# Kernel tuning notes

Hardware: AMD Instinct MI355X
Metric: run time of the kernel (lower is better)

Reference implementation:

```python
import jax, jax.numpy as jnp
import numpy as np

B, H, W = 16, 16, 16
DIM = 768
NH = 8
HD = DIM // NH
NEXP = 8
TOPK = 2
DSTATE = 1
DTRANK = 4
KDIR = 4


def setup_inputs() -> dict:
    key = jax.random.key(0)
    ks = jax.random.split(key, 16)
    s = 1.0 / float(np.sqrt(DIM))
    inp = {
        'x': jax.random.normal(ks[0], (B, H, W, DIM)),
        'sa_in_w': jax.random.normal(ks[1], (3 * DIM, DIM)) * s,
        'sa_in_b': jnp.zeros((3 * DIM,)),
        'sa_out_w': jax.random.normal(ks[2], (DIM, DIM)) * s,
        'sa_out_b': jnp.zeros((DIM,)),
        'ca_in_w': jax.random.normal(ks[3], (2 * DIM, DIM)) * s,
        'ca_in_b': jnp.zeros((2 * DIM,)),
        'expert_queries': jax.random.normal(ks[4], (NEXP, DIM)) * s,
        'e_in_w': jax.random.normal(ks[5], (NEXP, 2 * DIM, DIM)) * s,
        'e_in_b': jnp.zeros((NEXP, 2 * DIM)),
        'e_conv_w': jax.random.normal(ks[6], (NEXP, DIM, 1, 3, 3)) / 3.0,
        'e_conv_b': jnp.zeros((NEXP, DIM)),
        'e_xproj_w': jax.random.normal(ks[7], (NEXP, KDIR, DTRANK + 2 * DSTATE, DIM)) * s,
        'e_dtproj_w': jax.random.normal(ks[8], (NEXP, KDIR, DIM, DTRANK)) * 0.1,
        'e_dtproj_b': jax.random.uniform(ks[9], (NEXP, KDIR, DIM), minval=-4.0, maxval=-2.0),
        'e_Alog': jax.random.uniform(ks[10], (NEXP, KDIR, DIM, DSTATE), minval=0.0, maxval=1.0),
        'e_D': jnp.ones((NEXP, KDIR, DIM)),
        'e_ln_scale': jnp.ones((NEXP, DIM)),
        'e_ln_bias': jnp.zeros((NEXP, DIM)),
    }
    return {k: v.astype(jnp.float32) for k, v in inp.items()}


def _selective_scan(xs, Wx, Wdt, bdt, Alog, D):
    # xs: [B, L, d]; Wx: [R+2N, d]; Wdt: [d, R]; Alog: [d, N]; D: [d]
    dbl = jnp.einsum('bld,ed->ble', xs, Wx)
    dt = jax.nn.softplus(jnp.einsum('blr,dr->bld', dbl[..., :DTRANK], Wdt) + bdt)
    Bm = dbl[..., DTRANK:DTRANK + DSTATE]
    Cm = dbl[..., DTRANK + DSTATE:]
    A = -jnp.exp(Alog)  # [d, N]

    def step(h, t):
        dt_t, B_t, C_t, x_t = t  # [b,d],[b,N],[b,N],[b,d]
        h = jnp.exp(dt_t[:, :, None] * A) * h + (dt_t * x_t)[:, :, None] * B_t[:, None, :]
        return h, jnp.einsum('bdn,bn->bd', h, C_t)

    b, L, d = xs.shape
    h0 = jnp.zeros((b, d, DSTATE), xs.dtype)
    tm = lambda a: jnp.moveaxis(a, 1, 0)
    _, ys = jax.lax.scan(step, h0, (tm(dt), tm(Bm), tm(Cm), tm(xs)))
    return jnp.moveaxis(ys, 0, 1) + D * xs


def _expert(in_w, in_b, conv_w, conv_b, xproj_w, dtp_w, dtp_b, Alog, D, ln_s, ln_b, x):
    b = x.shape[0]
    xz = jnp.einsum('bhwc,oc->bhwo', x, in_w) + in_b
    xc, z = jnp.split(xz, 2, axis=-1)
    xn = jax.lax.conv_general_dilated(jnp.transpose(xc, (0, 3, 1, 2)), conv_w,
                                      (1, 1), ((1, 1), (1, 1)), feature_group_count=DIM)
    xc = jax.nn.silu(jnp.transpose(xn + conv_b[None, :, None, None], (0, 2, 3, 1)))
    L = H * W
    xh = xc.reshape(b, L, DIM)                              # row-major 'h'
    xv = jnp.transpose(xc, (0, 2, 1, 3)).reshape(b, L, DIM)  # col-major 'v'
    seqs = jnp.stack([xh, xh[:, ::-1], xv, xv[:, ::-1]])     # [4, b, L, d]
    ys = jax.vmap(_selective_scan)(seqs, xproj_w, dtp_w, dtp_b, Alog, D)
    yv = ys[2] + ys[3][:, ::-1]
    yv = jnp.transpose(yv.reshape(b, W, H, DIM), (0, 2, 1, 3)).reshape(b, L, DIM)
    y = (ys[0] + ys[1][:, ::-1] + yv).reshape(b, H, W, DIM)
    mu = y.mean(-1, keepdims=True)
    var = ((y - mu) ** 2).mean(-1, keepdims=True)
    y = (y - mu) * jax.lax.rsqrt(var + 1e-5) * ln_s + ln_b   # out_norm (LayerNorm)
    y = y * jax.nn.silu(z)
    return y.mean((1, 2))  # AdaptiveAvgPool2d((1,1)) -> [b, DIM]


def _forward(x, sa_in_w, sa_in_b, sa_out_w, sa_out_b, ca_in_w, ca_in_b, expert_queries,
             e_in_w, e_in_b, e_conv_w, e_conv_b, e_xproj_w, e_dtproj_w, e_dtproj_b,
             e_Alog, e_D, e_ln_scale, e_ln_bias):
    b = x.shape[0]
    L = H * W
    scale = 1.0 / float(np.sqrt(HD))
    xs = x.reshape(b, L, DIM)
    # spatial self-attention (eval mode: dropout off)
    qkv = xs @ sa_in_w.T + sa_in_b
    q, k, v = [a.reshape(b, L, NH, HD) for a in jnp.split(qkv, 3, -1)]
    att = jax.nn.softmax(jnp.einsum('bqhd,bkhd->bhqk', q, k) * scale, -1)
    ctx = jnp.einsum('bhqk,bkhd->bqhd', att, v).reshape(b, L, DIM) @ sa_out_w.T + sa_out_b
    # expert cross-attention: only head-averaged attention weights are used
    q2 = (ctx @ ca_in_w[:DIM].T + ca_in_b[:DIM]).reshape(b, L, NH, HD)
    k2 = (expert_queries @ ca_in_w[DIM:].T + ca_in_b[DIM:]).reshape(NEXP, NH, HD)
    aw = jax.nn.softmax(jnp.einsum('blhd,ehd->bhle', q2, k2) * scale, -1).mean(1)  # [b,L,E]
    gate = jax.nn.softmax(aw.mean(1), -1)  # [b, E]
    tk_scores, tk_idx = jax.lax.top_k(gate, TOPK)
    wgt = jax.nn.softmax(tk_scores, -1)
    # dense expert compute (all experts on all samples), then gather top-k
    all_out = jax.vmap(_expert, in_axes=(0,) * 11 + (None,))(
        e_in_w, e_in_b, e_conv_w, e_conv_b, e_xproj_w, e_dtproj_w, e_dtproj_b,
        e_Alog, e_D, e_ln_scale, e_ln_bias, x)  # [E, b, DIM]
    per_b = jnp.transpose(all_out, (1, 0, 2))  # [b, E, DIM]
    sel = jnp.take_along_axis(per_b, tk_idx[:, :, None], axis=1)  # [b, K, DIM]
    return jnp.sum(wgt[:, :, None] * sel, axis=1)  # [b, DIM]


def reference(x, sa_in_w, sa_in_b, sa_out_w, sa_out_b, ca_in_w, ca_in_b, expert_queries,
              e_in_w, e_in_b, e_conv_w, e_conv_b, e_xproj_w, e_dtproj_w, e_dtproj_b,
              e_Alog, e_D, e_ln_scale, e_ln_bias):
    return _forward(x, sa_in_w, sa_in_b, sa_out_w, sa_out_b, ca_in_w, ca_in_b, expert_queries,
                    e_in_w, e_in_b, e_conv_w, e_conv_b, e_xproj_w, e_dtproj_w, e_dtproj_b,
                    e_Alog, e_D, e_ln_scale, e_ln_bias)
```

## Files before the change

kernel.cpp:

```cpp
#include <hip/hip_runtime.h>
#include <hip/hip_bf16.h>


#define LTOK 256
#define DIMC 768

typedef unsigned short ushortt;
typedef __attribute__((ext_vector_type(8))) short bf16x8;
typedef __attribute__((ext_vector_type(4))) float f32x4;

#define LOG2E 1.44269504f
#define LN2   0.69314718f

__device__ __forceinline__ float fexp2(float x) { return __builtin_amdgcn_exp2f(x); }
__device__ __forceinline__ float flog2(float x) { return __builtin_amdgcn_logf(x); }

__device__ __forceinline__ ushortt f2b(float f) {
  union { float f; unsigned u; } c; c.f = f;
  unsigned r = (c.u + 0x7FFFu + ((c.u >> 16) & 1u)) >> 16;
  return (ushortt)r;
}

__global__ __launch_bounds__(256) void mk_mcast4(
    const float* __restrict__ s0, ushortt* __restrict__ d0,
    const float* __restrict__ s1, ushortt* __restrict__ d1,
    const float* __restrict__ s2, ushortt* __restrict__ d2,
    const float* __restrict__ s3, ushortt* __restrict__ d3)
{
  long g = (long)blockIdx.x * 256 + threadIdx.x;
  const float* s; ushortt* dst; long o;
  if (g < 786432)       { s = s0; dst = d0; o = g; }
  else if (g < 1228800) { s = s1; dst = d1; o = g - 786432; }
  else if (g < 1376256) { s = s2; dst = d2; o = g - 1228800; }
  else                  { s = s3; dst = d3; o = g - 1376256; }
  o <<= 2;
  float4 v = *(const float4*)(s + o);
  ushort4 w;
  w.x = f2b(v.x); w.y = f2b(v.y); w.z = f2b(v.z); w.w = f2b(v.w);
  *(ushort4*)(dst + o) = w;
}

__global__ __launch_bounds__(256) void mk_cast(const float* __restrict__ in,
                                               ushortt* __restrict__ outp, long n)
{
  long i = ((long)blockIdx.x * 256 + threadIdx.x) * 4;
  if (i + 3 < n) {
    float4 v = *(const float4*)(in + i);
    ushort4 o;
    o.x = f2b(v.x); o.y = f2b(v.y); o.z = f2b(v.z); o.w = f2b(v.w);
    *(ushort4*)(outp + i) = o;
  }
}

__global__ __launch_bounds__(256) void mk_mfma(
    const ushortt* __restrict__ A, const ushortt* __restrict__ B,
    const float* __restrict__ bias, void* __restrict__ C,
    int K, int lda, int ldb, int ldc,
    int zdiv, long sA1, long sA2, long sB1, long sB2, long sC1, long sC2,
    long sBias,
    const int* __restrict__ pairExp, int tilesN,
    int outBf, int splitN, void* __restrict__ C2, int ldc2, int outBf2, int c2vt)
{
  int z = blockIdx.y;
  long aoff, boff, coff, biasoff = 0;
  if (pairExp) {
    int e = pairExp[z];
    aoff = (long)(z >> 1) * sA1; boff = (long)e * sB1;
    coff = (long)z * sC1; biasoff = (long)e * sBias;
  } else {
    int z1 = z / zdiv, z2 = z - z1 * zdiv;
    aoff = (long)z1 * sA1 + (long)z2 * sA2;
    boff = (long)z1 * sB1 + (long)z2 * sB2;
    coff = (long)z1 * sC1 + (long)z2 * sC2;
  }
  int tile = blockIdx.x;
  int tm = tile / tilesN, tn = tile - tm * tilesN;
  long m0 = (long)tm << 7, n0 = (long)tn << 7;

  __shared__ ushortt As[128][40];
  __shared__ ushortt Bs[128][40];

  int tid = threadIdx.x;
  int lane = tid & 63, wvi = tid >> 6;
  int wr = wvi >> 1, wc = wvi & 1;
  int lm = lane & 15, lg = lane >> 4;

  f32x4 zero4 = {0.f, 0.f, 0.f, 0.f};
  f32x4 acc[4][4];
#pragma unroll
  for (int i = 0; i < 4; i++)
#pragma unroll
    for (int j = 0; j < 4; j++) acc[i][j] = zero4;

  const ushortt* Ab = A + aoff;
  const ushortt* Bb = B + boff;

  for (int k0 = 0; k0 < K; k0 += 32) {
#pragma unroll
    for (int h = 0; h < 2; h++) {
      int q = tid + h * 256;
      int row = q >> 2, ck = (q & 3) << 3;
      *(uint4*)&As[row][ck] = *(const uint4*)(Ab + (m0 + row) * lda + k0 + ck);
      *(uint4*)&Bs[row][ck] = *(const uint4*)(Bb + (n0 + row) * ldb + k0 + ck);
    }
    __syncthreads();
    bf16x8 af[4], bfr[4];
#pragma unroll
    for (int i = 0; i < 4; i++)
      af[i] = *(const bf16x8*)&As[wr * 64 + i * 16 + lm][lg << 3];
#pragma unroll
    for (int j = 0; j < 4; j++)
      bfr[j] = *(const bf16x8*)&Bs[wc * 64 + j * 16 + lm][lg << 3];
#pragma unroll
    for (int i = 0; i < 4; i++)
#pragma unroll
      for (int j = 0; j < 4; j++)
        acc[i][j] = __builtin_amdgcn_mfma_f32_16x16x32_bf16(af[i], bfr[j], acc[i][j], 0, 0, 0);
    __syncthreads();
  }

#pragma unroll
  for (int mt = 0; mt < 4; mt++) {
#pragma unroll
    for (int nt = 0; nt < 4; nt++) {
      long grow = m0 + wr * 64 + mt * 16 + lg * 4;
      long gcol = n0 + wc * 64 + nt * 16 + lm;
      float bv = bias ? bias[biasoff + gcol] : 0.f;
      if ((int)gcol < splitN) {
#pragma unroll
        for (int r = 0; r < 4; r++) {
          float v = acc[mt][nt][r] + bv;
          long idx = coff + (grow + r) * ldc + gcol;
          if (outBf) ((ushortt*)C)[idx] = f2b(v);
          else ((float*)C)[idx] = v;
        }
      } else if (c2vt) {
        int cc = (int)gcol - splitN;
        int hh = cc / 96, jj = cc - hh * 96;
#pragma unroll
        for (int r = 0; r < 4; r++) {
          float v = acc[mt][nt][r] + bv;
          long gr = grow + r;
          long b = gr >> 8, t = gr & 255;
          long idx = (((b * 8 + hh) * 128 + jj) << 8) + t;
          ((ushortt*)C2)[idx] = f2b(v);
        }
      } else {
        long col = gcol - splitN;
#pragma unroll
        for (int r = 0; r < 4; r++) {
          float v = acc[mt][nt][r] + bv;
          long idx = coff + (grow + r) * ldc2 + col;
          if (outBf2) ((ushortt*)C2)[idx] = f2b(v);
          else ((float*)C2)[idx] = v;
        }
      }
    }
  }
}

__global__ __launch_bounds__(256) void mk_gemm(
    const float* __restrict__ A, const float* __restrict__ B,
    const float* __restrict__ bias, float* __restrict__ C,
    int M, int N, int K, int lda, int ldb, int ldc, int tilesN)
{
  int tile = blockIdx.x;
  int tm = tile / tilesN, tn = tile - tm * tilesN;
  int m0 = tm << 6, n0 = tn << 6;

  __shared__ float As[16][68];
  __shared__ float Bs[16][68];

  int tid = threadIdx.x;
  int tx = tid & 15, ty = tid >> 4;
  int lrow = tid >> 2;
  int lk = (tid & 3) << 2;

  float acc[4][4];
#pragma unroll
  for (int i = 0; i < 4; i++)
#pragma unroll
    for (int j = 0; j < 4; j++) acc[i][j] = 0.f;

  for (int k0 = 0; k0 < K; k0 += 16) {
    {
      int gm = m0 + lrow;
      float4 v = {0.f, 0.f, 0.f, 0.f};
      if (gm < M) v = *(const float4*)(A + (long)gm * lda + (k0 + lk));
      As[lk + 0][lrow] = v.x; As[lk + 1][lrow] = v.y;
      As[lk + 2][lrow] = v.z; As[lk + 3][lrow] = v.w;
    }
    {
      int gn = n0 + lrow;
      float4 v = {0.f, 0.f, 0.f, 0.f};
      if (gn < N) v = *(const float4*)(B + (long)gn * ldb + (k0 + lk));
      Bs[lk + 0][lrow] = v.x; Bs[lk + 1][lrow] = v.y;
      Bs[lk + 2][lrow] = v.z; Bs[lk + 3][lrow] = v.w;
    }
    __syncthreads();
#pragma unroll
    for (int kk = 0; kk < 16; kk++) {
      float4 a = *(const float4*)&As[kk][ty << 2];
      float4 b = *(const float4*)&Bs[kk][tx << 2];
      acc[0][0] += a.x * b.x; acc[0][1] += a.x * b.y; acc[0][2] += a.x * b.z; acc[0][3] += a.x * b.w;
      acc[1][0] += a.y * b.x; acc[1][1] += a.y * b.y; acc[1][2] += a.y * b.z; acc[1][3] += a.y * b.w;
      acc[2][0] += a.z * b.x; acc[2][1] += a.z * b.y; acc[2][2] += a.z * b.z; acc[2][3] += a.z * b.w;
      acc[3][0] += a.w * b.x; acc[3][1] += a.w * b.y; acc[3][2] += a.w * b.z; acc[3][3] += a.w * b.w;
    }
    __syncthreads();
  }

#pragma unroll
  for (int i = 0; i < 4; i++) {
    int gm = m0 + (ty << 2) + i;
    if (gm >= M) continue;
#pragma unroll
    for (int j = 0; j < 4; j++) {
      int gn = n0 + (tx << 2) + j;
      if (gn >= N) continue;
      float v = acc[i][j];
      if (bias) v += bias[gn];
      C[(long)gm * ldc + gn] = v;
    }
  }
}

__global__ __launch_bounds__(256) void mk_softmax(const float* __restrict__ scores,
                                                  ushortt* __restrict__ att, float scale)
{
  int row = (blockIdx.x << 2) + (threadIdx.x >> 6);
  int lane = threadIdx.x & 63;
  const float* p = scores + (long)row * 256 + (lane << 2);
  float4 v = *(const float4*)p;
  float m = fmaxf(fmaxf(v.x, v.y), fmaxf(v.z, v.w));
#pragma unroll
  for (int o = 32; o; o >>= 1) m = fmaxf(m, __shfl_xor(m, o, 64));
  float sl = scale * LOG2E;
  v.x = fexp2(sl * (v.x - m));
  v.y = fexp2(sl * (v.y - m));
  v.z = fexp2(sl * (v.z - m));
  v.w = fexp2(sl * (v.w - m));
  float s = v.x + v.y + v.z + v.w;
#pragma unroll
  for (int o = 32; o; o >>= 1) s += __shfl_xor(s, o, 64);
  float r = 1.f / s;
  ushort4 o4;
  o4.x = f2b(v.x * r); o4.y = f2b(v.y * r); o4.z = f2b(v.z * r); o4.w = f2b(v.w * r);
  *(ushort4*)(att + (long)row * 256 + (lane << 2)) = o4;
}

__global__ __launch_bounds__(256) void mk_gates(const float* __restrict__ q2,
                                                const float* __restrict__ k2,
                                                float* __restrict__ gacc)
{
  __shared__ float k2p[8 * 808];
  int b = blockIdx.x >> 4, q = blockIdx.x & 15;
  for (int i = threadIdx.x; i < 6144; i += 256) {
    int e = i / 768, rem = i - e * 768;
    int h = rem / 96, j = rem - h * 96;
    k2p[e * 808 + h * 100 + j] = k2[i];
  }
  __syncthreads();
  const float scale = 0.10206207261596577f;
  int wid = threadIdx.x >> 6, lane = threadIdx.x & 63;
  int h = lane >> 3, e = lane & 7;
  const float* kp = &k2p[e * 808 + h * 100];
  float accL = 0.f;
#pragma unroll
  for (int ti = 0; ti < 4; ti++) {
    int l = q * 16 + wid * 4 + ti;
    const float* qh = q2 + ((long)b * LTOK + l) * DIMC + h * 96;
    float sum = 0.f;
#pragma unroll
    for (int j = 0; j < 96; j += 4) {
      float4 qv = *(const float4*)(qh + j);
      float4 kv = *(const float4*)(kp + j);
      sum += qv.x * kv.x + qv.y * kv.y + qv.z * kv.z + qv.w * kv.w;
    }
    float s = sum * scale;
    float mx = s;
#pragma unroll
    for (int o = 1; o <= 4; o <<= 1) mx = fmaxf(mx, __shfl_xor(mx, o, 64));
    float ex = fexp2((s - mx) * LOG2E);
    float se = ex;
#pragma unroll
    for (int o = 1; o <= 4; o <<= 1) se += __shfl_xor(se, o, 64);
    accL += ex / se;
  }
#pragma unroll
  for (int o = 8; o <= 32; o <<= 1) accL += __shfl_xor(accL, o, 64);
  __shared__ float red[4][8];
  if (lane < 8) red[wid][lane] = accL;
  __syncthreads();
  if (threadIdx.x < 8) {
    float v = red[0][threadIdx.x] + red[1][threadIdx.x] +
              red[2][threadIdx.x] + red[3][threadIdx.x];
    atomicAdd(&gacc[b * 8 + threadIdx.x], v);
  }
}

__global__ __launch_bounds__(64) void mk_gatetop(const float* __restrict__ gacc,
                                                 int* __restrict__ pe,
                                                 float* __restrict__ pw)
{
  int b = threadIdx.x;
  if (b >= 16) return;
  float g[8];
  for (int e = 0; e < 8; e++) g[e] = gacc[b * 8 + e] * (1.f / (8.f * 256.f));
  float mx = g[0];
  for (int e = 1; e < 8; e++) mx = fmaxf(mx, g[e]);
  float se = 0.f;
  for (int e = 0; e < 8; e++) { g[e] = expf(g[e] - mx); se += g[e]; }
  for (int e = 0; e < 8; e++) g[e] /= se;
  int i0 = 0;
  for (int e = 1; e < 8; e++) if (g[e] > g[i0]) i0 = e;
  int i1 = (i0 == 0) ? 1 : 0;
  for (int e = 0; e < 8; e++) if (e != i0 && g[e] > g[i1]) i1 = e;
  float w0 = 1.f / (1.f + expf(g[i1] - g[i0]));
  pe[2 * b] = i0; pe[2 * b + 1] = i1;
  pw[2 * b] = w0; pw[2 * b + 1] = 1.f - w0;
}

__global__ __launch_bounds__(768) void mk_conv(const float* __restrict__ xzx,
                                               const float* __restrict__ cw,
                                               const float* __restrict__ cb,
                                               const int* __restrict__ pe,
                                               float* __restrict__ xc)
{
  int blk = blockIdx.x;
  int p = blk >> 8, t = blk & 255;
  int e = pe[p];
  int h = t >> 4, w = t & 15;
  int c = threadIdx.x;
  const float* wp = cw + ((long)e * DIMC + c) * 9;
  float acc = cb[e * DIMC + c];
#pragma unroll
  for (int dh = 0; dh < 3; dh++) {
    int hh = h + dh - 1;
    if (hh < 0 || hh > 15) continue;
#pragma unroll
    for (int dw = 0; dw < 3; dw++) {
      int ww = w + dw - 1;
      if (ww < 0 || ww > 15) continue;
      acc += xzx[((long)p * LTOK + hh * 16 + ww) * DIMC + c] * wp[dh * 3 + dw];
    }
  }
  xc[((long)p * LTOK + t) * DIMC + c] = acc / (1.f + fexp2(-acc * LOG2E));
}

__device__ __forceinline__ int tmap(int dir, int s) {
  if (dir == 0) return s;
  if (dir == 1) return 255 - s;
  if (dir == 2) return ((s & 15) << 4) | (s >> 4);
  int u = 255 - s;
  return ((u & 15) << 4) | (u >> 4);
}

__global__ __launch_bounds__(256) void mk_dbl(const float* __restrict__ xc,
                                              const float* __restrict__ xproj,
                                              const int* __restrict__ pe,
                                              float* __restrict__ dblm)
{
  int p = blockIdx.x >> 6;
  int tq = blockIdx.x & 63;
  int wid = threadIdx.x >> 6, lane = threadIdx.x & 63;
  int m = tq * 4 + wid;
  int e = pe[p];
  const float* xr = xc + ((long)p * LTOK + m) * DIMC;
  const float* wb = xproj + (long)e * 24 * DIMC;
  float4 xv[3];
#pragma unroll
  for (int j = 0; j < 3; j++) xv[j] = *(const float4*)(xr + j * 256 + lane * 4);
  float acc[24];
#pragma unroll
  for (int r = 0; r < 24; r++) {
    const float* wr = wb + r * DIMC;
    float s = 0.f;
#pragma unroll
    for (int j = 0; j < 3; j++) {
      float4 wv = *(const float4*)(wr + j * 256 + lane * 4);
      s += xv[j].x * wv.x + xv[j].y * wv.y + xv[j].z * wv.z + xv[j].w * wv.w;
    }
    acc[r] = s;
  }
#pragma unroll
  for (int r = 0; r < 24; r++)
#pragma unroll
    for (int o = 32; o; o >>= 1) acc[r] += __shfl_xor(acc[r], o, 64);
  if (lane == 0) {
    float* o = dblm + ((long)p * LTOK + m) * 32;
#pragma unroll
    for (int r = 0; r < 24; r++) o[(r / 6) * 8 + (r - (r / 6) * 6)] = acc[r];
  }
}

__global__ __launch_bounds__(512, 6) void mk_scan(const float* __restrict__ xc,
                                               const float* __restrict__ dblm,
                                               const float* __restrict__ dtw,
                                               const float* __restrict__ dtb,
                                               const float* __restrict__ Alog,
                                               const float* __restrict__ Dp,
                                               const int* __restrict__ pe,
                                               float* __restrict__ yac)
{
  __shared__ __attribute__((aligned(16))) float dbS[256 * 32];
  __shared__ float yS[256 * 17];
  __shared__ float ahS[32][16][2];
  __shared__ float dsum[16];
  int blk = blockIdx.x;
  int p = blk / 48, cg = blk - p * 48;
  int c0 = cg << 4;
  int e = pe[p];
  int tid = threadIdx.x;
  {
    const float4* src = (const float4*)(dblm + (long)p * LTOK * 32);
    for (int i = tid; i < 2048; i += 512) {
      int t = i >> 3, c4 = i & 7;
      int rot = ((t >> 5) ^ (t >> 1)) & 7;
      *(float4*)&dbS[t * 32 + (((c4 ^ rot) & 7) << 2)] = src[i];
    }
  }
  for (int i = tid; i < 256 * 17; i += 512) yS[i] = 0.f;
  if (tid < 16) {
    float s = 0.f;
#pragma unroll
    for (int dd = 0; dd < 4; dd++) s += Dp[(long)(e * 4 + dd) * DIMC + c0 + tid];
    dsum[tid] = s;
  }
  __syncthreads();

  int c = tid & 15;
  int rr = tid >> 4;
  int seg = rr & 7;
  int dir = rr >> 3;
  int d = c0 + c;
  const float* xcp = xc + (long)p * LTOK * DIMC + d;
  long pb = (long)(e * 4 + dir) * DIMC + d;
  float4 wv = *(const float4*)(dtw + pb * 4);
  float bdt = dtb[pb];
  float Ad = -fexp2(Alog[pb] * LOG2E);
  int t0 = seg << 5;
  int stp = (dir == 0) ? 1 : (dir == 1) ? -1 : (dir == 2) ? 16 : -16;
  int dslot = dir * 2, bslot = dir * 2 + 1;

  float h = 0.f, ap = 1.f;
  for (int tb = 0; tb < 32; tb += 8) {
    int mb = tmap(dir, t0 + tb);
#pragma unroll
    for (int i = 0; i < 8; i++) {
      int mm = mb + i * stp;
      int rot = ((mm >> 5) ^ (mm >> 1)) & 7;
      float4 dv = *(const float4*)&dbS[mm * 32 + (((dslot ^ rot) & 7) << 2)];
      float Bv = dbS[mm * 32 + (((bslot ^ rot) & 7) << 2)];
      float xl = (wv.x * dv.x + wv.y * dv.y + wv.z * dv.z + wv.w * dv.w + bdt) * LOG2E;
      float te = fexp2(xl);
      float g = flog2(1.f + te);
      g = (xl > 86.f) ? xl : g;
      float de = fexp2(g * Ad);
      float xv = xcp[(long)mm * DIMC];
      h = de * h + (g * LN2) * xv * Bv;
      ap *= de;
    }
  }
  ahS[rr][c][0] = ap;
  ahS[rr][c][1] = h;
  __syncthreads();

  float hh = 0.f;
  {
    int base = dir << 3;
    float av[8], hv[8];
#pragma unroll
    for (int j = 0; j < 8; j++) {
      av[j] = ahS[base + j][c][0];
      hv[j] = ahS[base + j][c][1];
    }
#pragma unroll
    for (int j = 0; j < 7; j++)
      if (j < seg) hh = av[j] * hh + hv[j];
  }

  for (int tb = 0; tb < 32; tb += 8) {
    int mb = tmap(dir, t0 + tb);
#pragma unroll
    for (int i = 0; i < 8; i++) {
      int mm = mb + i * stp;
      int rot = ((mm >> 5) ^ (mm >> 1)) & 7;
      float4 dv = *(const float4*)&dbS[mm * 32 + (((dslot ^ rot) & 7) << 2)];
      float2 bc = *(const float2*)&dbS[mm * 32 + (((bslot ^ rot) & 7) << 2)];
      float xl = (wv.x * dv.x + wv.y * dv.y + wv.z * dv.z + wv.w * dv.w + bdt) * LOG2E;
      float te = fexp2(xl);
      float g = flog2(1.f + te);
      g = (xl > 86.f) ? xl : g;
      float de = fexp2(g * Ad);
      float xv = xcp[(long)mm * DIMC];
      hh = de * hh + (g * LN2) * xv * bc.x;
      atomicAdd(&yS[mm * 17 + c], hh * bc.y);
    }
  }
  __syncthreads();

  const float* xcb = xc + (long)p * LTOK * DIMC + c0;
  float* yp = yac + (long)p * LTOK * DIMC + c0;
  for (int i = tid; i < 4096; i += 512) {
    int t = i >> 4, cz = i & 15;
    yp[(long)t * DIMC + cz] = yS[t * 17 + cz] + xcb[(long)t * DIMC + cz] * dsum[cz];
  }
}

__global__ __launch_bounds__(256) void mk_lnfin(const float* __restrict__ yac,
                                                const float* __restrict__ xzz,
                                                const float* __restrict__ lns,
                                                const float* __restrict__ lnb,
                                                const int* __restrict__ pe,
                                                float* __restrict__ eo)
{
  int blk = blockIdx.x;
  int p = blk >> 4, ts = blk & 15;
  int e = pe[p];
  int tid = threadIdx.x;
  int wid = tid >> 6, lane = tid & 63;
  float ls[12], lb[12], acc[12];
#pragma unroll
  for (int i = 0; i < 12; i++) {
    int d = i * 64 + lane;
    ls[i] = lns[e * DIMC + d];
    lb[i] = lnb[e * DIMC + d];
    acc[i] = 0.f;
  }
#pragma unroll
  for (int tt = 0; tt < 4; tt++) {
    int t = ts * 16 + wid * 4 + tt;
    const float* yr = yac + ((long)p * LTOK + t) * DIMC;
    const float* zr = xzz + ((long)p * LTOK + t) * DIMC;
    float v[12];
    float s = 0.f;
#pragma unroll
    for (int i = 0; i < 12; i++) { v[i] = yr[i * 64 + lane]; s += v[i]; }
#pragma unroll
    for (int o = 32; o; o >>= 1) s += __shfl_xor(s, o, 64);
    float mu = s * (1.f / 768.f);
    float sq = 0.f;
#pragma unroll
    for (int i = 0; i < 12; i++) { float dlt = v[i] - mu; sq += dlt * dlt; }
#pragma unroll
    for (int o = 32; o; o >>= 1) sq += __shfl_xor(sq, o, 64);
    float rs = rsqrtf(sq * (1.f / 768.f) + 1e-5f);
#pragma unroll
    for (int i = 0; i < 12; i++) {
      float y = (v[i] - mu) * rs * ls[i] + lb[i];
      float z = zr[i * 64 + lane];
      y *= z / (1.f + fexp2(-z * LOG2E));
      acc[i] += y;
    }
  }
  __shared__ float sacc[768];
  for (int j = tid; j < 768; j += 256) sacc[j] = 0.f;
  __syncthreads();
#pragma unroll
  for (int i = 0; i < 12; i++) atomicAdd(&sacc[i * 64 + lane], acc[i]);
  __syncthreads();
  for (int j = tid; j < 768; j += 256) atomicAdd(&eo[(long)p * DIMC + j], sacc[j]);
}

__global__ __launch_bounds__(768) void mk_out(const float* __restrict__ eo,
                                              const float* __restrict__ pw,
                                              float* __restrict__ out)
{
  int b = blockIdx.x, d = threadIdx.x;
  float v = pw[2 * b] * eo[(long)(2 * b) * DIMC + d] +
            pw[2 * b + 1] * eo[(long)(2 * b + 1) * DIMC + d];
  out[b * DIMC + d] = v * (1.f / 256.f);
}

extern "C" void kernel_launch(void* const* d_in, const int* in_sizes, int n_in,
                              void* d_out, int out_size, void* d_ws, size_t ws_size,
                              hipStream_t stream)
{
  const float* x        = (const float*)d_in[0];
  const float* sa_in_w  = (const float*)d_in[1];
  const float* sa_in_b  = (const float*)d_in[2];
  const float* sa_out_w = (const float*)d_in[3];
  const float* sa_out_b = (const float*)d_in[4];
  const float* ca_in_w  = (const float*)d_in[5];
  const float* ca_in_b  = (const float*)d_in[6];
  const float* eq       = (const float*)d_in[7];
  const float* e_in_w   = (const float*)d_in[8];
  const float* e_in_b   = (const float*)d_in[9];
  const float* e_conv_w = (const float*)d_in[10];
  const float* e_conv_b = (const float*)d_in[11];
  const float* e_xproj  = (const float*)d_in[12];
  const float* e_dtw    = (const float*)d_in[13];
  const float* e_dtb    = (const float*)d_in[14];
  const float* e_Alog   = (const float*)d_in[15];
  const float* e_D      = (const float*)d_in[16];
  const float* e_lns    = (const float*)d_in[17];
  const float* e_lnb    = (const float*)d_in[18];
  float* out = (float*)d_out;

  float* ws = (float*)d_ws;
  ushortt* qk_b   = (ushortt*)(ws + 0);
  float*   scores = ws + 6291456;
  ushortt* dump_b = (ushortt*)(ws + 6291456);
  ushortt* ctxa_b = (ushortt*)(ws + 7864320);
  ushortt* att_b  = (ushortt*)(ws + 14680064);
  ushortt* vt_b   = (ushortt*)(ws + 18874368);
  ushortt* xb     = (ushortt*)(ws + 20971520);
  ushortt* wqkv_b = (ushortt*)(ws + 22544384);
  ushortt* saow_b = (ushortt*)(ws + 23429120);
  ushortt* caw_b  = (ushortt*)(ws + 23724032);
  ushortt* ctx_b  = (ushortt*)(ws + 0);
  float*   q2     = ws + 1572864;
  float*   k2     = ws + 25165824;
  int*     pe     = (int*)(ws + 25171968);
  float*   pw     = ws + 25172000;
  float*   eo     = ws + 25172032;
  float*   gacc   = ws + 25393216;
  float*   xz_x   = ws + 0;
  float*   xz_z   = ws + 6291456;
  ushortt* ew_b   = (ushortt*)(ws + 12582912);
  float*   xc     = ws + 12582912;
  float*   yac    = ws + 18874368;
  float*   dblm   = ws + 0;

  const float scale = 0.10206207261596577f;

  mk_mcast4<<<5952, 256, 0, stream>>>(x, xb, sa_in_w, wqkv_b, sa_out_w, saow_b,
                                      ca_in_w, caw_b);
  mk_mfma<<<dim3(576, 1), 256, 0, stream>>>(xb, wqkv_b, sa_in_b, qk_b,
      768, 768, 768, 1536, 1, 0, 0, 0, 0, 0, 0, 0, nullptr, 18,
      1, 1536, vt_b, 0, 1, 1);
  mk_mfma<<<dim3(4, 128), 256, 0, stream>>>(qk_b, qk_b + 768, nullptr, scores,
      96, 1536, 1536, 256, 8, 393216, 96, 393216, 96, 524288, 65536, 0, nullptr, 2,
      0, 1 << 30, nullptr, 0, 0, 0);
  mk_softmax<<<8192, 256, 0, stream>>>(scores, att_b, scale);
  mk_mfma<<<dim3(2, 128), 256, 0, stream>>>(att_b, vt_b, nullptr, ctxa_b,
      256, 256, 256, 768, 8, 524288, 65536, 262144, 32768, 196608, 96, 0, nullptr, 1,
      1, 96, dump_b, 32, 1, 0);
  mk_cast<<<9216, 256, 0, stream>>>(e_in_w, ew_b, 9437184);
  mk_mfma<<<dim3(192, 1), 256, 0, stream>>>(ctxa_b, saow_b, sa_out_b, ctx_b,
      768, 768, 768, 768, 1, 0, 0, 0, 0, 0, 0, 0, nullptr, 6,
      1, 1 << 30, nullptr, 0, 0, 0);
  mk_mfma<<<dim3(192, 1), 256, 0, stream>>>(ctx_b, caw_b, ca_in_b, q2,
      768, 768, 768, 768, 1, 0, 0, 0, 0, 0, 0, 0, nullptr, 6,
      0, 1 << 30, nullptr, 0, 0, 0);
  mk_gemm<<<dim3(12, 1), 256, 0, stream>>>(eq, ca_in_w + 589824, ca_in_b + 768, k2,
      8, 768, 768, 768, 768, 768, 12);
  (void)hipMemsetAsync(gacc, 0, 128 * sizeof(float), stream);
  (void)hipMemsetAsync(eo, 0, 24576 * sizeof(float), stream);
  mk_gates<<<256, 256, 0, stream>>>(q2, k2, gacc);
  mk_gatetop<<<1, 64, 0, stream>>>(gacc, pe, pw);
  mk_mfma<<<dim3(24, 32), 256, 0, stream>>>(xb, ew_b, e_in_b, xz_x,
      768, 768, 768, 768, 1, 196608, 0, 1179648, 0, 196608, 0, 1536, pe, 12,
      0, 768, xz_z, 768, 0, 0);
  mk_conv<<<32 * 256, 768, 0, stream>>>(xz_x, e_conv_w, e_conv_b, pe, xc);
  mk_dbl<<<2048, 256, 0, stream>>>(xc, e_xproj, pe, dblm);
  mk_scan<<<1536, 512, 0, stream>>>(xc, dblm, e_dtw, e_dtb, e_Alog, e_D, pe, yac);
  mk_lnfin<<<512, 256, 0, stream>>>(yac, xz_z, e_lns, e_lnb, pe, eo);
  mk_out<<<16, 768, 0, stream>>>(eo, pw, out);

  (void)in_sizes; (void)n_in; (void)out_size; (void)ws_size;
}
```

Baseline: 629.2 us.

## Split scan into 16 segments per direction with staged x and parallel prefix combine

The selective-scan kernel now runs 1024 threads per block, giving each direction 16 chunks of 16 timesteps instead of 8 chunks of 32. This halves the serial recurrence length per thread. The xc tile is staged once into shared memory so both scan passes and the final D-skip read it there instead of making strided global loads. The chunk carry combine becomes a Hillis-Steele log-step scan over shared memory. In exchange it adds more shared memory, several extra block barriers, and lower register and occupancy headroom under the (1024,4) launch bounds.

```diff
diff --git a/kernel.cpp b/kernel.cpp
--- a/kernel.cpp
+++ b/kernel.cpp
@@ -394,7 +394,7 @@
   }
 }
 
-__global__ __launch_bounds__(512, 6) void mk_scan(const float* __restrict__ xc,
+__global__ __launch_bounds__(1024, 4) void mk_scan(const float* __restrict__ xc,
                                                const float* __restrict__ dblm,
                                                const float* __restrict__ dtw,
                                                const float* __restrict__ dtb,
@@ -405,7 +405,8 @@
 {
   __shared__ __attribute__((aligned(16))) float dbS[256 * 32];
   __shared__ float yS[256 * 17];
-  __shared__ float ahS[32][16][2];
+  __shared__ float xS[256 * 17];
+  __shared__ float ahS[64][16][2];
   __shared__ float dsum[16];
   int blk = blockIdx.x;
   int p = blk / 48, cg = blk - p * 48;
@@ -414,13 +415,20 @@
   int tid = threadIdx.x;
   {
     const float4* src = (const float4*)(dblm + (long)p * LTOK * 32);
-    for (int i = tid; i < 2048; i += 512) {
+    for (int i = tid; i < 2048; i += 1024) {
       int t = i >> 3, c4 = i & 7;
       int rot = ((t >> 5) ^ (t >> 1)) & 7;
       *(float4*)&dbS[t * 32 + (((c4 ^ rot) & 7) << 2)] = src[i];
     }
   }
-  for (int i = tid; i < 256 * 17; i += 512) yS[i] = 0.f;
+  {
+    const float* xcp0 = xc + (long)p * LTOK * DIMC + c0;
+    int t = tid >> 2, c4 = (tid & 3) << 2;
+    float4 v = *(const float4*)(xcp0 + (long)t * DIMC + c4);
+    float* xd = &xS[t * 17 + c4];
+    xd[0] = v.x; xd[1] = v.y; xd[2] = v.z; xd[3] = v.w;
+  }
+  for (int i = tid; i < 256 * 17; i += 1024) yS[i] = 0.f;
   if (tid < 16) {
     float s = 0.f;
 #pragma unroll
@@ -431,80 +439,71 @@
 
   int c = tid & 15;
   int rr = tid >> 4;
-  int seg = rr & 7;
-  int dir = rr >> 3;
+  int seg = rr & 15;
+  int dir = rr >> 4;
   int d = c0 + c;
-  const float* xcp = xc + (long)p * LTOK * DIMC + d;
   long pb = (long)(e * 4 + dir) * DIMC + d;
   float4 wv = *(const float4*)(dtw + pb * 4);
   float bdt = dtb[pb];
   float Ad = -fexp2(Alog[pb] * LOG2E);
-  int t0 = seg << 5;
+  int t0 = seg << 4;
   int stp = (dir == 0) ? 1 : (dir == 1) ? -1 : (dir == 2) ? 16 : -16;
+  int mb = tmap(dir, t0);
   int dslot = dir * 2, bslot = dir * 2 + 1;
 
   float h = 0.f, ap = 1.f;
-  for (int tb = 0; tb < 32; tb += 8) {
-    int mb = tmap(dir, t0 + tb);
-#pragma unroll
-    for (int i = 0; i < 8; i++) {
-      int mm = mb + i * stp;
-      int rot = ((mm >> 5) ^ (mm >> 1)) & 7;
-      float4 dv = *(const float4*)&dbS[mm * 32 + (((dslot ^ rot) & 7) << 2)];
-      float Bv = dbS[mm * 32 + (((bslot ^ rot) & 7) << 2)];
-      float xl = (wv.x * dv.x + wv.y * dv.y + wv.z * dv.z + wv.w * dv.w + bdt) * LOG2E;
-      float te = fexp2(xl);
-      float g = flog2(1.f + te);
-      g = (xl > 86.f) ? xl : g;
-      float de = fexp2(g * Ad);
-      float xv = xcp[(long)mm * DIMC];
-      h = de * h + (g * LN2) * xv * Bv;
-      ap *= de;
-    }
+#pragma unroll
+  for (int i = 0; i < 16; i++) {
+    int mm = mb + i * stp;
+    int rot = ((mm >> 5) ^ (mm >> 1)) & 7;
+    float4 dv = *(const float4*)&dbS[mm * 32 + (((dslot ^ rot) & 7) << 2)];
+    float Bv = dbS[mm * 32 + (((bslot ^ rot) & 7) << 2)];
+    float xl = (wv.x * dv.x + wv.y * dv.y + wv.z * dv.z + wv.w * dv.w + bdt) * LOG2E;
+    float te = fexp2(xl);
+    float g = flog2(1.f + te);
+    g = (xl > 86.f) ? xl : g;
+    float de = fexp2(g * Ad);
+    float xv = xS[mm * 17 + c];
+    h = de * h + (g * LN2) * xv * Bv;
+    ap *= de;
   }
   ahS[rr][c][0] = ap;
   ahS[rr][c][1] = h;
   __syncthreads();
 
-  float hh = 0.f;
-  {
-    int base = dir << 3;
-    float av[8], hv[8];
-#pragma unroll
-    for (int j = 0; j < 8; j++) {
-      av[j] = ahS[base + j][c][0];
-      hv[j] = ahS[base + j][c][1];
-    }
-#pragma unroll
-    for (int j = 0; j < 7; j++)
-      if (j < seg) hh = av[j] * hh + hv[j];
-  }
-
-  for (int tb = 0; tb < 32; tb += 8) {
-    int mb = tmap(dir, t0 + tb);
-#pragma unroll
-    for (int i = 0; i < 8; i++) {
-      int mm = mb + i * stp;
-      int rot = ((mm >> 5) ^ (mm >> 1)) & 7;
-      float4 dv = *(const float4*)&dbS[mm * 32 + (((dslot ^ rot) & 7) << 2)];
-      float2 bc = *(const float2*)&dbS[mm * 32 + (((bslot ^ rot) & 7) << 2)];
-      float xl = (wv.x * dv.x + wv.y * dv.y + wv.z * dv.z + wv.w * dv.w + bdt) * LOG2E;
-      float te = fexp2(xl);
-      float g = flog2(1.f + te);
-      g = (xl > 86.f) ? xl : g;
-      float de = fexp2(g * Ad);
-      float xv = xcp[(long)mm * DIMC];
-      hh = de * hh + (g * LN2) * xv * bc.x;
-      atomicAdd(&yS[mm * 17 + c], hh * bc.y);
-    }
+#pragma unroll
+  for (int k = 1; k < 16; k <<= 1) {
+    float sa = ahS[rr][c][0], sh = ahS[rr][c][1];
+    float oa = 1.f, oh = 0.f;
+    if (seg >= k) { oa = ahS[rr - k][c][0]; oh = ahS[rr - k][c][1]; }
+    __syncthreads();
+    ahS[rr][c][0] = sa * oa;
+    ahS[rr][c][1] = sa * oh + sh;
+    __syncthreads();
+  }
+  float hh = (seg == 0) ? 0.f : ahS[rr - 1][c][1];
+
+#pragma unroll
+  for (int i = 0; i < 16; i++) {
+    int mm = mb + i * stp;
+    int rot = ((mm >> 5) ^ (mm >> 1)) & 7;
+    float4 dv = *(const float4*)&dbS[mm * 32 + (((dslot ^ rot) & 7) << 2)];
+    float2 bc = *(const float2*)&dbS[mm * 32 + (((bslot ^ rot) & 7) << 2)];
+    float xl = (wv.x * dv.x + wv.y * dv.y + wv.z * dv.z + wv.w * dv.w + bdt) * LOG2E;
+    float te = fexp2(xl);
+    float g = flog2(1.f + te);
+    g = (xl > 86.f) ? xl : g;
+    float de = fexp2(g * Ad);
+    float xv = xS[mm * 17 + c];
+    hh = de * hh + (g * LN2) * xv * bc.x;
+    atomicAdd(&yS[mm * 17 + c], hh * bc.y);
   }
   __syncthreads();
 
-  const float* xcb = xc + (long)p * LTOK * DIMC + c0;
   float* yp = yac + (long)p * LTOK * DIMC + c0;
-  for (int i = tid; i < 4096; i += 512) {
+  for (int i = tid; i < 4096; i += 1024) {
     int t = i >> 4, cz = i & 15;
-    yp[(long)t * DIMC + cz] = yS[t * 17 + cz] + xcb[(long)t * DIMC + cz] * dsum[cz];
+    yp[(long)t * DIMC + cz] = yS[t * 17 + cz] + xS[t * 17 + cz] * dsum[cz];
   }
 }
 
@@ -655,7 +654,7 @@
       0, 768, xz_z, 768, 0, 0);
   mk_conv<<<32 * 256, 768, 0, stream>>>(xz_x, e_conv_w, e_conv_b, pe, xc);
   mk_dbl<<<2048, 256, 0, stream>>>(xc, e_xproj, pe, dblm);
-  mk_scan<<<1536, 512, 0, stream>>>(xc, dblm, e_dtw, e_dtb, e_Alog, e_D, pe, yac);
+  mk_scan<<<1536, 1024, 0, stream>>>(xc, dblm, e_dtw, e_dtb, e_Alog, e_D, pe, yac);
   mk_lnfin<<<512, 256, 0, stream>>>(yac, xz_z, e_lns, e_lnb, pe, eo);
   mk_out<<<16, 768, 0, stream>>>(eo, pw, out);
 
```

Result: slower. 662.2 us (+5.2%).

## Store scan projections in direction-ordered scan layout to simplify LDS access

Applied to the files above, without the earlier changes.

The x-projection kernel now writes dt and B/C values into per-direction arrays ordered by scan step and interleaved by segment, instead of per-token rows with a swizzle. The scan kernel copies these contiguously into separate LDS buffers and reads them with a fixed stride, removing the per-step XOR swizzle and tmap-based address math. It also folds LOG2E into the dt weights and bias, and pads the y accumulator rows to 18 with an offset to reduce bank conflicts on the atomic adds. The producer writes are now scattered, and the new layout must match the segment mapping exactly.

```diff
diff --git a/kernel.cpp b/kernel.cpp
--- a/kernel.cpp
+++ b/kernel.cpp
@@ -388,9 +388,17 @@
 #pragma unroll
     for (int o = 32; o; o >>= 1) acc[r] += __shfl_xor(acc[r], o, 64);
   if (lane == 0) {
-    float* o = dblm + ((long)p * LTOK + m) * 32;
-#pragma unroll
-    for (int r = 0; r < 24; r++) o[(r / 6) * 8 + (r - (r / 6) * 6)] = acc[r];
+    float* o = dblm + (long)p * 6144;
+#pragma unroll
+    for (int dd = 0; dd < 4; dd++) {
+      int s = tmap(dd, m);
+      int ss = ((s & 31) << 3) | (s >> 5);
+      float* oa = o + dd * 1024 + ss * 4;
+      oa[0] = acc[dd * 6 + 0]; oa[1] = acc[dd * 6 + 1];
+      oa[2] = acc[dd * 6 + 2]; oa[3] = acc[dd * 6 + 3];
+      float* ob = o + 4096 + dd * 512 + ss * 2;
+      ob[0] = acc[dd * 6 + 4]; ob[1] = acc[dd * 6 + 5];
+    }
   }
 }
 
@@ -403,8 +411,9 @@
                                                const int* __restrict__ pe,
                                                float* __restrict__ yac)
 {
-  __shared__ __attribute__((aligned(16))) float dbS[256 * 32];
-  __shared__ float yS[256 * 17];
+  __shared__ __attribute__((aligned(16))) float dtS[4096];
+  __shared__ __attribute__((aligned(16))) float bcS[2048];
+  __shared__ float yS[256 * 18];
   __shared__ float ahS[32][16][2];
   __shared__ float dsum[16];
   int blk = blockIdx.x;
@@ -413,14 +422,12 @@
   int e = pe[p];
   int tid = threadIdx.x;
   {
-    const float4* src = (const float4*)(dblm + (long)p * LTOK * 32);
-    for (int i = tid; i < 2048; i += 512) {
-      int t = i >> 3, c4 = i & 7;
-      int rot = ((t >> 5) ^ (t >> 1)) & 7;
-      *(float4*)&dbS[t * 32 + (((c4 ^ rot) & 7) << 2)] = src[i];
-    }
-  }
-  for (int i = tid; i < 256 * 17; i += 512) yS[i] = 0.f;
+    const float4* src = (const float4*)(dblm + (long)p * 6144);
+    float4* dA = (float4*)dtS;
+    for (int i = tid; i < 1024; i += 512) dA[i] = src[i];
+    if (tid < 512) ((float4*)bcS)[tid] = src[1024 + tid];
+  }
+  for (int i = tid; i < 256 * 18; i += 512) yS[i] = 0.f;
   if (tid < 16) {
     float s = 0.f;
 #pragma unroll
@@ -437,30 +444,27 @@
   const float* xcp = xc + (long)p * LTOK * DIMC + d;
   long pb = (long)(e * 4 + dir) * DIMC + d;
   float4 wv = *(const float4*)(dtw + pb * 4);
-  float bdt = dtb[pb];
+  wv.x *= LOG2E; wv.y *= LOG2E; wv.z *= LOG2E; wv.w *= LOG2E;
+  float bdt = dtb[pb] * LOG2E;
   float Ad = -fexp2(Alog[pb] * LOG2E);
   int t0 = seg << 5;
-  int stp = (dir == 0) ? 1 : (dir == 1) ? -1 : (dir == 2) ? 16 : -16;
-  int dslot = dir * 2, bslot = dir * 2 + 1;
+  const float* dtP = &dtS[(dir << 10) + (seg << 2)];
+  const float* bcP = &bcS[(dir << 9) + (seg << 1)];
 
   float h = 0.f, ap = 1.f;
-  for (int tb = 0; tb < 32; tb += 8) {
-    int mb = tmap(dir, t0 + tb);
-#pragma unroll
-    for (int i = 0; i < 8; i++) {
-      int mm = mb + i * stp;
-      int rot = ((mm >> 5) ^ (mm >> 1)) & 7;
-      float4 dv = *(const float4*)&dbS[mm * 32 + (((dslot ^ rot) & 7) << 2)];
-      float Bv = dbS[mm * 32 + (((bslot ^ rot) & 7) << 2)];
-      float xl = (wv.x * dv.x + wv.y * dv.y + wv.z * dv.z + wv.w * dv.w + bdt) * LOG2E;
-      float te = fexp2(xl);
-      float g = flog2(1.f + te);
-      g = (xl > 86.f) ? xl : g;
-      float de = fexp2(g * Ad);
-      float xv = xcp[(long)mm * DIMC];
-      h = de * h + (g * LN2) * xv * Bv;
-      ap *= de;
-    }
+#pragma unroll
+  for (int i = 0; i < 32; i++) {
+    float4 dv = *(const float4*)(dtP + i * 32);
+    float2 bc = *(const float2*)(bcP + i * 16);
+    int mm = tmap(dir, t0 + i);
+    float xv = xcp[(long)mm * DIMC];
+    float xl = wv.x * dv.x + wv.y * dv.y + wv.z * dv.z + wv.w * dv.w + bdt;
+    float te = fexp2(xl);
+    float g = flog2(1.f + te);
+    g = (xl > 86.f) ? xl : g;
+    float de = fexp2(g * Ad);
+    h = de * h + (g * LN2 * bc.x) * xv;
+    ap *= de;
   }
   ahS[rr][c][0] = ap;
   ahS[rr][c][1] = h;
@@ -480,23 +484,19 @@
       if (j < seg) hh = av[j] * hh + hv[j];
   }
 
-  for (int tb = 0; tb < 32; tb += 8) {
-    int mb = tmap(dir, t0 + tb);
-#pragma unroll
-    for (int i = 0; i < 8; i++) {
-      int mm = mb + i * stp;
-      int rot = ((mm >> 5) ^ (mm >> 1)) & 7;
-      float4 dv = *(const float4*)&dbS[mm * 32 + (((dslot ^ rot) & 7) << 2)];
-      float2 bc = *(const float2*)&dbS[mm * 32 + (((bslot ^ rot) & 7) << 2)];
-      float xl = (wv.x * dv.x + wv.y * dv.y + wv.z * dv.z + wv.w * dv.w + bdt) * LOG2E;
-      float te = fexp2(xl);
-      float g = flog2(1.f + te);
-      g = (xl > 86.f) ? xl : g;
-      float de = fexp2(g * Ad);
-      float xv = xcp[(long)mm * DIMC];
-      hh = de * hh + (g * LN2) * xv * bc.x;
-      atomicAdd(&yS[mm * 17 + c], hh * bc.y);
-    }
+#pragma unroll
+  for (int i = 0; i < 32; i++) {
+    float4 dv = *(const float4*)(dtP + i * 32);
+    float2 bc = *(const float2*)(bcP + i * 16);
+    int mm = tmap(dir, t0 + i);
+    float xv = xcp[(long)mm * DIMC];
+    float xl = wv.x * dv.x + wv.y * dv.y + wv.z * dv.z + wv.w * dv.w + bdt;
+    float te = fexp2(xl);
+    float g = flog2(1.f + te);
+    g = (xl > 86.f) ? xl : g;
+    float de = fexp2(g * Ad);
+    hh = de * hh + (g * LN2 * bc.x) * xv;
+    atomicAdd(&yS[mm * 18 + c + (((mm >> 5) & 1) << 1)], hh * bc.y);
   }
   __syncthreads();
 
@@ -504,7 +504,8 @@
   float* yp = yac + (long)p * LTOK * DIMC + c0;
   for (int i = tid; i < 4096; i += 512) {
     int t = i >> 4, cz = i & 15;
-    yp[(long)t * DIMC + cz] = yS[t * 17 + cz] + xcb[(long)t * DIMC + cz] * dsum[cz];
+    yp[(long)t * DIMC + cz] = yS[t * 18 + cz + (((t >> 5) & 1) << 1)] +
+        xcb[(long)t * DIMC + cz] * dsum[cz];
   }
 }
 
```

Result: slower. 847.6 us (+34.7%).
